# Optimization experiments

Measured on AMD Instinct MI355X. Metric: run time of the kernel, lower is better.

Reference implementation:

```python
import jax, jax.numpy as jnp
from jax import lax
import numpy as np

DN = ('NCHW', 'OIHW', 'NCHW')

def conv(x, w, b, stride=1, groups=1):
    y = lax.conv_general_dilated(x, w, (stride, stride), 'SAME',
                                 feature_group_count=groups, dimension_numbers=DN)
    return y + b[None, :, None, None]

def sep_conv(x, dw, pw, pb):
    # depthwise 3x3 -> pointwise 1x1 -> ReLU (BN is frozen at identity)
    y = lax.conv_general_dilated(x, dw, (1, 1), 'SAME',
                                 feature_group_count=x.shape[1], dimension_numbers=DN)
    return jax.nn.relu(conv(y, pw, pb))

def up2(x):
    return jnp.repeat(jnp.repeat(x, 2, axis=2), 2, axis=3)

def down2(x):
    return lax.reduce_window(x, -jnp.inf, lax.max, (1, 1, 2, 2), (1, 1, 2, 2), 'VALID')

def fuse(w, *xs):
    # fast normalized fusion
    w = jax.nn.relu(w)
    w = w / (jnp.sum(w) + 1e-4)
    out = w[0] * xs[0]
    for i in range(1, len(xs)):
        out = out + w[i] * xs[i]
    return out

def bifpn_layer(ps, dw, pw, pb, fw2, fw3):
    p3, p4, p5, p6, p7 = ps
    p6t = sep_conv(fuse(fw2[0], p6, up2(p7)),  dw[0], pw[0], pb[0])
    p5t = sep_conv(fuse(fw2[1], p5, up2(p6t)), dw[1], pw[1], pb[1])
    p4t = sep_conv(fuse(fw2[2], p4, up2(p5t)), dw[2], pw[2], pb[2])
    p3o = sep_conv(fuse(fw2[3], p3, up2(p4t)), dw[3], pw[3], pb[3])
    p4o = sep_conv(fuse(fw3[0], p4, p4t, down2(p3o)), dw[4], pw[4], pb[4])
    p5o = sep_conv(fuse(fw3[1], p5, p5t, down2(p4o)), dw[5], pw[5], pb[5])
    p6o = sep_conv(fuse(fw3[2], p6, p6t, down2(p5o)), dw[6], pw[6], pb[6])
    p7o = sep_conv(fuse(fw2[4], p7, down2(p6o)),      dw[7], pw[7], pb[7])
    return [p3o, p4o, p5o, p6o, p7o]

def make_anchors(img_size):
    # RetinaNet-style anchors: pyramid levels 3..7, 3 scales x 3 ratios
    ratios = np.array([0.5, 1.0, 2.0])
    scales = 2.0 ** (np.arange(3) / 3.0)
    boxes_all = []
    for lvl in range(3, 8):
        stride = 2 ** lvl
        size = 2 ** (lvl + 2)
        fs = img_size // stride
        ws = (size * scales[None, :] / np.sqrt(ratios)[:, None]).reshape(-1)  # [9]
        hs = (size * scales[None, :] * np.sqrt(ratios)[:, None]).reshape(-1)
        ctr = (np.arange(fs) + 0.5) * stride
        gy, gx = np.meshgrid(ctr, ctr, indexing='ij')
        centers = np.stack([gx, gy], -1).reshape(-1, 1, 2)      # [HW,1,2] (x,y)
        wh = np.stack([ws, hs], -1)[None]                       # [1,9,2]
        boxes = np.concatenate([centers - wh / 2, centers + wh / 2], -1).reshape(-1, 4)
        boxes_all.append(boxes)
    return jnp.asarray(np.concatenate(boxes_all, 0), jnp.float32)

def run_head(p, tw, tb, ow, ob, out_ch):
    x = p
    for i in range(tw.shape[0]):
        x = jax.nn.relu(conv(x, tw[i], tb[i]))
    y = conv(x, ow, ob)                                  # [B, 9*out_ch, H, W]
    B, _, H, W = y.shape
    return y.transpose(0, 2, 3, 1).reshape(B, H * W * 9, out_ch)

def setup_inputs() -> dict:
    key = jax.random.key(0)
    ks = iter(jax.random.split(key, 64))
    B, W, NC, ST, D = 4, 88, 90, 3, 4
    chans = [40, 80, 112, 192, 320]
    hw = [64, 32, 16, 8, 4]
    inp = {}
    for i, (c, h) in enumerate(zip(chans, hw)):
        inp[f'c{i+3}'] = jax.random.normal(next(ks), (B, c, h, h), jnp.float32)
        inp[f'lat_w{i+3}'] = jax.random.normal(next(ks), (W, c, 1, 1), jnp.float32) * 0.05
        inp[f'lat_b{i+3}'] = jnp.zeros((W,), jnp.float32)
    inp['bif_dw'] = jax.random.normal(next(ks), (ST, 8, W, 1, 3, 3), jnp.float32) * 0.1
    inp['bif_pw'] = jax.random.normal(next(ks), (ST, 8, W, W, 1, 1), jnp.float32) * 0.05
    inp['bif_pb'] = jnp.zeros((ST, 8, W), jnp.float32)
    inp['bif_fw2'] = jnp.ones((ST, 5, 2), jnp.float32)
    inp['bif_fw3'] = jnp.ones((ST, 3, 3), jnp.float32)
    inp['reg_tw'] = jax.random.normal(next(ks), (D, W, W, 3, 3), jnp.float32) * 0.03
    inp['reg_tb'] = jnp.zeros((D, W), jnp.float32)
    inp['reg_ow'] = jax.random.normal(next(ks), (36, W, 3, 3), jnp.float32) * 0.01
    inp['reg_ob'] = jnp.zeros((36,), jnp.float32)
    inp['cls_tw'] = jax.random.normal(next(ks), (D, W, W, 3, 3), jnp.float32) * 0.03
    inp['cls_tb'] = jnp.zeros((D, W), jnp.float32)
    inp['cls_ow'] = jax.random.normal(next(ks), (9 * NC, W, 3, 3), jnp.float32) * 0.01
    inp['cls_ob'] = jnp.full((9 * NC,), -np.log((1.0 - 0.01) / 0.01), jnp.float32)
    inp['img_size'] = 512
    return inp

def reference(c3, c4, c5, c6, c7,
              lat_w3, lat_b3, lat_w4, lat_b4, lat_w5, lat_b5,
              lat_w6, lat_b6, lat_w7, lat_b7,
              bif_dw, bif_pw, bif_pb, bif_fw2, bif_fw3,
              reg_tw, reg_tb, reg_ow, reg_ob,
              cls_tw, cls_tb, cls_ow, cls_ob,
              img_size):
    num_classes = cls_ow.shape[0] // 9
    ps = [conv(c3, lat_w3, lat_b3), conv(c4, lat_w4, lat_b4), conv(c5, lat_w5, lat_b5),
          conv(c6, lat_w6, lat_b6), conv(c7, lat_w7, lat_b7)]
    for s in range(bif_dw.shape[0]):
        ps = bifpn_layer(ps, bif_dw[s], bif_pw[s], bif_pb[s], bif_fw2[s], bif_fw3[s])
    regression = jnp.concatenate([run_head(p, reg_tw, reg_tb, reg_ow, reg_ob, 4) for p in ps], axis=1)
    classification = jnp.concatenate(
        [jax.nn.sigmoid(run_head(p, cls_tw, cls_tb, cls_ow, cls_ob, num_classes)) for p in ps], axis=1)
    anchors = make_anchors(int(img_size))
    return classification, regression, anchors
```

## Files before the change

### kernel.cpp

```cpp
#include <hip/hip_runtime.h>
#include <math.h>

#define TPB 256
static inline int cdiv(int a, int b) { return (a + b - 1) / b; }

typedef __attribute__((ext_vector_type(8))) short short8;
typedef __attribute__((ext_vector_type(4))) float floatx4;

__device__ __forceinline__ float bf2f(ushort u) {
    union { unsigned int u; float f; } v; v.u = ((unsigned int)u) << 16; return v.f;
}
__device__ __forceinline__ ushort f2bf(float f) {
    union { float f; unsigned int u; } v; v.f = f;
    unsigned int r = (v.u + 0x7FFFu + ((v.u >> 16) & 1u)) >> 16;
    return (ushort)r;
}

#define CONC_ROWS 21824
__device__ __forceinline__ void lvl_of(int row, int& lvl, int& base) {
    lvl = 0; base = 0;
    if (row >= 16384) { lvl = 1; base = 16384; }
    if (row >= 20480) { lvl = 2; base = 20480; }
    if (row >= 21504) { lvl = 3; base = 21504; }
    if (row >= 21760) { lvl = 4; base = 21760; }
}
__constant__ int LOFFc[5] = {0, 36864, 46080, 48384, 48960};

__global__ void pack3_k(const float* __restrict__ w, ushort* __restrict__ Bp,
                        int Ntot, int CO, int total) {
    int idx = blockIdx.x * blockDim.x + threadIdx.x;
    if (idx >= total) return;
    int j = idx & 7; int t = idx >> 3;
    int n = t % Ntot; t /= Ntot;
    int g = t & 3; t >>= 2;
    int ks = t % 3; int tap = t / 3;
    int ci = ks * 32 + g * 8 + j;
    float v = (ci < 88 && n < CO) ? w[((size_t)n * 88 + ci) * 9 + tap] : 0.f;
    Bp[idx] = f2bf(v);
}

__global__ void pack_tw8_k(const float* __restrict__ rw, const float* __restrict__ cw,
                           ushort* __restrict__ Bp) {
    int idx = blockIdx.x * blockDim.x + threadIdx.x;
    if (idx >= 8 * 82944) return;
    int i = idx / 82944; int r = idx - i * 82944;
    const float* w = (i < 4) ? rw + (size_t)i * 69696 : cw + (size_t)(i - 4) * 69696;
    int j = r & 7; int t = r >> 3;
    int n = t % 96; t /= 96;
    int g = t & 3; t >>= 2;
    int ks = t % 3; int tap = t / 3;
    int ci = ks * 32 + g * 8 + j;
    float v = (ci < 88 && n < 88) ? w[((size_t)n * 88 + ci) * 9 + tap] : 0.f;
    Bp[idx] = f2bf(v);
}

__global__ void pack_pw_all_k(const float* __restrict__ pw, ushort* __restrict__ Bp,
                              int total) {
    int idx = blockIdx.x * blockDim.x + threadIdx.x;
    if (idx >= total) return;
    int cid = idx / 9216; int r = idx - cid * 9216;
    int j = r & 7; int t = r >> 3;
    int n = t % 96; t /= 96;
    int g = t & 3; int ks = t >> 2;
    int ci = ks * 32 + g * 8 + j;
    float v = (ci < 88 && n < 88) ? pw[(size_t)cid * 7744 + n * 88 + ci] : 0.f;
    Bp[idx] = f2bf(v);
}

__global__ void pack_lat_k(const float* __restrict__ w3, const float* __restrict__ w4,
                           const float* __restrict__ w5, const float* __restrict__ w6,
                           const float* __restrict__ w7, ushort* __restrict__ Bp) {
    int idx = blockIdx.x * blockDim.x + threadIdx.x;
    if (idx >= 76800) return;
    int l, off;
    if (idx < 6144)       { l = 0; off = 0; }
    else if (idx < 15360) { l = 1; off = 6144; }
    else if (idx < 27648) { l = 2; off = 15360; }
    else if (idx < 46080) { l = 3; off = 27648; }
    else                  { l = 4; off = 46080; }
    const float* w = l == 0 ? w3 : l == 1 ? w4 : l == 2 ? w5 : l == 3 ? w6 : w7;
    const int cins[5] = {40, 80, 112, 192, 320};
    int Cin = cins[l];
    int r = idx - off;
    int j = r & 7; int t = r >> 3;
    int n = t % 96; t /= 96;
    int g = t & 3; int ks = t >> 2;
    int ci = ks * 32 + g * 8 + j;
    float v = (ci < Cin && n < 88) ? w[(size_t)n * Cin + ci] : 0.f;
    Bp[idx] = f2bf(v);
}

__global__ __launch_bounds__(256)
void lateral_mfma_k(const float* __restrict__ x, const ushort* __restrict__ Bp,
                    const float* __restrict__ bias, ushort* __restrict__ out,
                    int Cin, int KS, int logHH) {
    __shared__ ushort As[64 * 40];
    int tid = threadIdx.x;
    int m0 = blockIdx.x * 64;
    int lane = tid & 63, l15 = lane & 15, g = (lane >> 4) & 3;
    int wave = tid >> 6, wm = wave & 1, wn = wave >> 1;
    floatx4 acc[2][3];
#pragma unroll
    for (int a = 0; a < 2; ++a)
#pragma unroll
        for (int b = 0; b < 3; ++b) acc[a][b] = (floatx4){0.f, 0.f, 0.f, 0.f};
    const short8* Bq = (const short8*)Bp;

    int p = m0 + lane;
    int n = p >> logHH, pp = p & ((1 << logHH) - 1);
    const float* xp = x + (((size_t)n * Cin) << logHH) + pp;

    for (int ks = 0; ks < KS; ++ks) {
        __syncthreads();
#pragma unroll
        for (int it = 0; it < 8; ++it) {
            int ciL = (tid >> 6) + it * 4;
            int ci = ks * 32 + ciL;
            float v = (ci < Cin) ? xp[(size_t)ci << logHH] : 0.f;
            As[lane * 40 + ciL] = f2bf(v);
        }
        __syncthreads();
        short8 a0 = *(const short8*)(&As[(wm * 32 + l15) * 40 + g * 8]);
        short8 a1 = *(const short8*)(&As[(wm * 32 + 16 + l15) * 40 + g * 8]);
        int bbase = (ks * 4 + g) * 96 + wn * 48 + l15;
#pragma unroll
        for (int nf = 0; nf < 3; ++nf) {
            short8 b = Bq[bbase + nf * 16];
            acc[0][nf] = __builtin_amdgcn_mfma_f32_16x16x32_bf16(a0, b, acc[0][nf], 0, 0, 0);
            acc[1][nf] = __builtin_amdgcn_mfma_f32_16x16x32_bf16(a1, b, acc[1][nf], 0, 0, 0);
        }
    }
    float bc[3];
#pragma unroll
    for (int nf = 0; nf < 3; ++nf) {
        int c = wn * 48 + nf * 16 + l15;
        bc[nf] = (c < 88) ? bias[c] : 0.f;
    }
#pragma unroll
    for (int mf = 0; mf < 2; ++mf)
#pragma unroll
        for (int r = 0; r < 4; ++r) {
            int pl = m0 + wm * 32 + mf * 16 + g * 4 + r;
#pragma unroll
            for (int nf = 0; nf < 3; ++nf) {
                int c = wn * 48 + nf * 16 + l15;
                out[(size_t)pl * 96 + c] = f2bf(acc[mf][nf][r] + bc[nf]);
            }
        }
}

template <int MODE>
__global__ __launch_bounds__(256, 2)
void sepconv_k(const ushort* __restrict__ a, const ushort* __restrict__ bsrc,
               const ushort* __restrict__ csrc, const float* __restrict__ fw,
               const float* __restrict__ dww, const ushort* __restrict__ Bp,
               const float* __restrict__ pbias, ushort* __restrict__ out,
               int logW) {
    __shared__ ushort Fs[195 * 104];
    __shared__ ushort Ds[64 * 104];
    __shared__ ushort Dwb[108 * 8];
    int tid = threadIdx.x;
    int W = 1 << logW, HH = W * W, log2HH = 2 * logW;
    int Mlv = 4 * HH;
    int HB = W + 1;
    int RS = 64 + 2 * HB;
    int pl0 = blockIdx.x * 64;
    float w0 = fmaxf(fw[0], 0.f), w1 = fmaxf(fw[1], 0.f);
    float w2 = (MODE == 2) ? fmaxf(fw[2], 0.f) : 0.f;
    float inv = 1.f / (w0 + w1 + w2 + 1e-4f);
    float w0i = w0 * inv, w1i = w1 * inv, w2i = w2 * inv;

    if (tid < 13) *(uint4*)(&Fs[194 * 104 + tid * 8]) = (uint4){0u, 0u, 0u, 0u};
    for (int i = tid; i < 108; i += 256) {
        int cg = i / 9, tap = i - cg * 9;
        ushort tmp[8];
#pragma unroll
        for (int j = 0; j < 8; ++j) {
            int c = cg * 8 + j;
            tmp[j] = (c < 88) ? f2bf(dww[c * 9 + tap]) : (ushort)0;
        }
        *(uint4*)(&Dwb[i * 8]) = *(uint4*)tmp;
    }
    for (int i = tid; i < RS * 12; i += 256) {
        int row = i / 12, cg = i - row * 12;
        int pl = pl0 - HB + row;
        uint4 res = {0u, 0u, 0u, 0u};
        if (pl >= 0 && pl < Mlv) {
            int n = pl >> log2HH, pp = pl & (HH - 1);
            int y = pp >> logW, x = pp & (W - 1);
            uint4 av = *(const uint4*)(a + (size_t)pl * 96 + cg * 8);
            const ushort* au = (const ushort*)&av;
            float f[8];
            if (MODE == 0) {
                int Wh = W >> 1;
                int bp = (n << (log2HH - 2)) + (y >> 1) * Wh + (x >> 1);
                uint4 bv = *(const uint4*)(bsrc + (size_t)bp * 96 + cg * 8);
                const ushort* bu = (const ushort*)&bv;
#pragma unroll
                for (int j = 0; j < 8; ++j)
                    f[j] = w0i * bf2f(au[j]) + w1i * bf2f(bu[j]);
            } else {
                int W2 = W << 1;
                const ushort* q = (MODE == 1 ? bsrc : csrc) +
                    ((size_t)((n << (log2HH + 2)) + (2 * y) * W2 + 2 * x)) * 96 + cg * 8;
                uint4 q0 = *(const uint4*)(q);
                uint4 q1 = *(const uint4*)(q + 96);
                uint4 q2 = *(const uint4*)(q + (size_t)W2 * 96);
                uint4 q3 = *(const uint4*)(q + (size_t)W2 * 96 + 96);
                const ushort* u0 = (const ushort*)&q0; const ushort* u1 = (const ushort*)&q1;
                const ushort* u2 = (const ushort*)&q2; const ushort* u3 = (const ushort*)&q3;
                if (MODE == 1) {
#pragma unroll
                    for (int j = 0; j < 8; ++j) {
                        float m = fmaxf(fmaxf(bf2f(u0[j]), bf2f(u1[j])),
                                        fmaxf(bf2f(u2[j]), bf2f(u3[j])));
                        f[j] = w0i * bf2f(au[j]) + w1i * m;
                    }
                } else {
                    uint4 b2v = *(const uint4*)(bsrc + (size_t)pl * 96 + cg * 8);
                    const ushort* b2u = (const ushort*)&b2v;
#pragma unroll
                    for (int j = 0; j < 8; ++j) {
                        float m = fmaxf(fmaxf(bf2f(u0[j]), bf2f(u1[j])),
                                        fmaxf(bf2f(u2[j]), bf2f(u3[j])));
                        f[j] = w0i * bf2f(au[j]) + w1i * bf2f(b2u[j]) + w2i * m;
                    }
                }
            }
            ushort tmp[8];
#pragma unroll
            for (int j = 0; j < 8; ++j) tmp[j] = f2bf(f[j]);
            res = *(uint4*)tmp;
        }
        *(uint4*)(&Fs[row * 104 + cg * 8]) = res;
    }
    __syncthreads();
    for (int i = tid; i < 768; i += 256) {
        int row = i / 12, cg = i - row * 12;
        int pl = pl0 + row;
        int pp = pl & (HH - 1);
        int y = pp >> logW, x = pp & (W - 1);
        float acc8[8] = {0.f, 0.f, 0.f, 0.f, 0.f, 0.f, 0.f, 0.f};
        if (cg < 11) {
#pragma unroll
            for (int tap = 0; tap < 9; ++tap) {
                int dy = tap / 3 - 1, dx = tap % 3 - 1;
                int sy = y + dy, sx = x + dx;
                bool pred = ((unsigned)sy < (unsigned)W) && ((unsigned)sx < (unsigned)W);
                int rsel = pred ? (row + HB + dy * W + dx) : 194;
                short8 fv = *(const short8*)(&Fs[rsel * 104 + cg * 8]);
                short8 wv = *(const short8*)(&Dwb[(cg * 9 + tap) * 8]);
#pragma unroll
                for (int j = 0; j < 8; ++j)
                    acc8[j] = fmaf(bf2f((ushort)fv[j]), bf2f((ushort)wv[j]), acc8[j]);
            }
        }
        ushort tmp[8];
#pragma unroll
        for (int j = 0; j < 8; ++j) tmp[j] = f2bf(acc8[j]);
        *(uint4*)(&Ds[row * 104 + cg * 8]) = *(uint4*)tmp;
    }
    __syncthreads();
    int lane = tid & 63, l15 = lane & 15, g = (lane >> 4) & 3;
    int wave = tid >> 6, wm = wave & 1, wn = wave >> 1;
    floatx4 acc[2][3];
#pragma unroll
    for (int aa = 0; aa < 2; ++aa)
#pragma unroll
        for (int bb = 0; bb < 3; ++bb) acc[aa][bb] = (floatx4){0.f, 0.f, 0.f, 0.f};
    const short8* Bq = (const short8*)Bp;
#pragma unroll
    for (int ks = 0; ks < 3; ++ks) {
        int k = ks * 32 + g * 8;
        short8 a0 = *(const short8*)(&Ds[(wm * 32 + l15) * 104 + k]);
        short8 a1 = *(const short8*)(&Ds[(wm * 32 + 16 + l15) * 104 + k]);
        int bbase = (ks * 4 + g) * 96 + wn * 48 + l15;
#pragma unroll
        for (int nf = 0; nf < 3; ++nf) {
            short8 b = Bq[bbase + nf * 16];
            acc[0][nf] = __builtin_amdgcn_mfma_f32_16x16x32_bf16(a0, b, acc[0][nf], 0, 0, 0);
            acc[1][nf] = __builtin_amdgcn_mfma_f32_16x16x32_bf16(a1, b, acc[1][nf], 0, 0, 0);
        }
    }
    float bc[3];
#pragma unroll
    for (int nf = 0; nf < 3; ++nf) {
        int c = wn * 48 + nf * 16 + l15;
        bc[nf] = (c < 88) ? pbias[c] : 0.f;
    }
#pragma unroll
    for (int mf = 0; mf < 2; ++mf)
#pragma unroll
        for (int r = 0; r < 4; ++r) {
            int pl = pl0 + wm * 32 + mf * 16 + g * 4 + r;
#pragma unroll
            for (int nf = 0; nf < 3; ++nf) {
                int c = wn * 48 + nf * 16 + l15;
                out[(size_t)pl * 96 + c] = f2bf(fmaxf(acc[mf][nf][r] + bc[nf], 0.f));
            }
        }
}

__global__ __launch_bounds__(256)
void tower_direct_k(const ushort* __restrict__ inR, const ushort* __restrict__ inC,
                    const ushort* __restrict__ BpR, const ushort* __restrict__ BpC,
                    const float* __restrict__ bR, const float* __restrict__ bC,
                    ushort* __restrict__ outR, ushort* __restrict__ outC,
                    const ushort* __restrict__ zb) {
    int head = blockIdx.y;
    const ushort* in = head ? inC : inR;
    const short8* Bq = (const short8*)(head ? BpC : BpR);
    const float* bias = head ? bC : bR;
    ushort* out = head ? outC : outR;
    int tid = threadIdx.x;
    int m0 = blockIdx.x * 64;
    int lvl, base; lvl_of(m0, lvl, base);
    int logW = 6 - lvl, W = 1 << logW, HH = W * W;
    int pl0 = m0 - base;
    int lane = tid & 63, l15 = lane & 15, g = (lane >> 4) & 3;
    int wave = tid >> 6, wm = wave & 1, wn = wave >> 1;
    int ym[2], xm[2];
    const ushort* pbase[2];
#pragma unroll
    for (int mf = 0; mf < 2; ++mf) {
        int pl = pl0 + wm * 32 + mf * 16 + l15;
        int pp = pl & (HH - 1);
        ym[mf] = pp >> logW; xm[mf] = pp & (W - 1);
        pbase[mf] = in + (size_t)(base + pl) * 96 + g * 8;
    }
    const ushort* zbg = zb + g * 8;
    floatx4 acc[2][3];
#pragma unroll
    for (int aa = 0; aa < 2; ++aa)
#pragma unroll
        for (int bb = 0; bb < 3; ++bb) acc[aa][bb] = (floatx4){0.f, 0.f, 0.f, 0.f};
#pragma unroll
    for (int tap = 0; tap < 9; ++tap) {
        const int dy = tap / 3 - 1, dx = tap % 3 - 1;
        int off96 = (dy * W + dx) * 96;
        const ushort* ap[2];
#pragma unroll
        for (int mf = 0; mf < 2; ++mf) {
            bool pred = ((unsigned)(ym[mf] + dy) < (unsigned)W) &&
                        ((unsigned)(xm[mf] + dx) < (unsigned)W);
            ap[mf] = pred ? (pbase[mf] + off96) : zbg;
        }
#pragma unroll
        for (int ks = 0; ks < 3; ++ks) {
            short8 a0 = *(const short8*)(ap[0] + ks * 32);
            short8 a1 = *(const short8*)(ap[1] + ks * 32);
            int bbase = ((tap * 3 + ks) * 4 + g) * 96 + wn * 48 + l15;
#pragma unroll
            for (int nf = 0; nf < 3; ++nf) {
                short8 b = Bq[bbase + nf * 16];
                acc[0][nf] = __builtin_amdgcn_mfma_f32_16x16x32_bf16(a0, b, acc[0][nf], 0, 0, 0);
                acc[1][nf] = __builtin_amdgcn_mfma_f32_16x16x32_bf16(a1, b, acc[1][nf], 0, 0, 0);
            }
        }
    }
    float bc[3];
#pragma unroll
    for (int nf = 0; nf < 3; ++nf) {
        int c = wn * 48 + nf * 16 + l15;
        bc[nf] = (c < 88) ? bias[c] : 0.f;
    }
#pragma unroll
    for (int mf = 0; mf < 2; ++mf)
#pragma unroll
        for (int r = 0; r < 4; ++r) {
            int pl = pl0 + wm * 32 + mf * 16 + g * 4 + r;
#pragma unroll
            for (int nf = 0; nf < 3; ++nf) {
                int c = wn * 48 + nf * 16 + l15;
                out[(size_t)(base + pl) * 96 + c] = f2bf(fmaxf(acc[mf][nf][r] + bc[nf], 0.f));
            }
        }
}

template <int OC, bool SIG>
__global__ __launch_bounds__(256)
void head_direct_k(const ushort* __restrict__ in, const ushort* __restrict__ Bp,
                   const float* __restrict__ bias, float* __restrict__ outb,
                   int Ntot, int C9, const ushort* __restrict__ zb) {
    int tid = threadIdx.x;
    int m0 = blockIdx.x * 64;
    int n0b = blockIdx.y * 96;
    int lvl, base; lvl_of(m0, lvl, base);
    int logW = 6 - lvl, W = 1 << logW, HH = W * W, log2HH = 2 * logW;
    int pl0 = m0 - base;
    int lane = tid & 63, l15 = lane & 15, g = (lane >> 4) & 3;
    int wave = tid >> 6, wm = wave & 1, wn = wave >> 1;
    int ym[2], xm[2];
    const ushort* pbase[2];
#pragma unroll
    for (int mf = 0; mf < 2; ++mf) {
        int pl = pl0 + wm * 32 + mf * 16 + l15;
        int pp = pl & (HH - 1);
        ym[mf] = pp >> logW; xm[mf] = pp & (W - 1);
        pbase[mf] = in + (size_t)(base + pl) * 96 + g * 8;
    }
    const ushort* zbg = zb + g * 8;
    floatx4 acc[2][3];
#pragma unroll
    for (int aa = 0; aa < 2; ++aa)
#pragma unroll
        for (int bb = 0; bb < 3; ++bb) acc[aa][bb] = (floatx4){0.f, 0.f, 0.f, 0.f};
    const short8* Bq = (const short8*)Bp;
#pragma unroll
    for (int tap = 0; tap < 9; ++tap) {
        const int dy = tap / 3 - 1, dx = tap % 3 - 1;
        int off96 = (dy * W + dx) * 96;
        const ushort* ap[2];
#pragma unroll
        for (int mf = 0; mf < 2; ++mf) {
            bool pred = ((unsigned)(ym[mf] + dy) < (unsigned)W) &&
                        ((unsigned)(xm[mf] + dx) < (unsigned)W);
            ap[mf] = pred ? (pbase[mf] + off96) : zbg;
        }
#pragma unroll
        for (int ks = 0; ks < 3; ++ks) {
            short8 a0 = *(const short8*)(ap[0] + ks * 32);
            short8 a1 = *(const short8*)(ap[1] + ks * 32);
            int bbase = ((tap * 3 + ks) * 4 + g) * Ntot + n0b + wn * 48 + l15;
#pragma unroll
            for (int nf = 0; nf < 3; ++nf) {
                short8 b = Bq[bbase + nf * 16];
                acc[0][nf] = __builtin_amdgcn_mfma_f32_16x16x32_bf16(a0, b, acc[0][nf], 0, 0, 0);
                acc[1][nf] = __builtin_amdgcn_mfma_f32_16x16x32_bf16(a1, b, acc[1][nf], 0, 0, 0);
            }
        }
    }
#pragma unroll
    for (int nf = 0; nf < 3; ++nf) {
        int c = n0b + wn * 48 + nf * 16 + l15;
        if (c >= C9) continue;
        float bcv = bias[c];
        int a = c / OC, kk = c - a * OC;
#pragma unroll
        for (int mf = 0; mf < 2; ++mf)
#pragma unroll
            for (int r = 0; r < 4; ++r) {
                int pl = pl0 + wm * 32 + mf * 16 + g * 4 + r;
                int n = pl >> log2HH, pp = pl & (HH - 1);
                float v = acc[mf][nf][r] + bcv;
                if (SIG) v = 1.f / (1.f + expf(-v));
                outb[((size_t)n * 49104 + LOFFc[lvl] + (size_t)pp * 9 + a) * OC + kk] = v;
            }
    }
}

__global__ void anchors_k(float* __restrict__ out, ushort* __restrict__ zb) {
    int idx = blockIdx.x * blockDim.x + threadIdx.x;
    if (idx < 48) ((unsigned int*)zb)[idx] = 0u;
    if (idx >= 49104) return;
    const int offs[6] = {0, 36864, 46080, 48384, 48960, 49104};
    int l = 0;
    while (idx >= offs[l + 1]) ++l;
    int j = idx - offs[l];
    int a = j % 9;
    int p = j / 9;
    int fs = 64 >> l;
    int stride = 8 << l;
    float size = (float)(32 << l);
    int ix = p % fs, iy = p / fs;
    float cx = (ix + 0.5f) * (float)stride;
    float cy = (iy + 0.5f) * (float)stride;
    const float scl[3] = {1.0f, 1.2599210498948732f, 1.5874010519681994f};
    const float sqr[3] = {0.7071067811865476f, 1.0f, 1.4142135623730951f};
    int r = a / 3, s = a % 3;
    float w = size * scl[s] / sqr[r];
    float h = size * scl[s] * sqr[r];
    float* o = out + (size_t)idx * 4;
    o[0] = cx - 0.5f * w;
    o[1] = cy - 0.5f * h;
    o[2] = cx + 0.5f * w;
    o[3] = cy + 0.5f * h;
}


extern "C" void kernel_launch(void* const* d_in, const int* in_sizes, int n_in,
                              void* d_out, int out_size, void* d_ws, size_t ws_size,
                              hipStream_t stream) {
    const float* c_in[5]  = {(const float*)d_in[0],  (const float*)d_in[3],
                             (const float*)d_in[6],  (const float*)d_in[9],
                             (const float*)d_in[12]};
    const float* lat_w[5] = {(const float*)d_in[1],  (const float*)d_in[4],
                             (const float*)d_in[7],  (const float*)d_in[10],
                             (const float*)d_in[13]};
    const float* lat_b[5] = {(const float*)d_in[2],  (const float*)d_in[5],
                             (const float*)d_in[8],  (const float*)d_in[11],
                             (const float*)d_in[14]};
    const float* bif_dw  = (const float*)d_in[15];
    const float* bif_pw  = (const float*)d_in[16];
    const float* bif_pb  = (const float*)d_in[17];
    const float* bif_fw2 = (const float*)d_in[18];
    const float* bif_fw3 = (const float*)d_in[19];
    const float* reg_tw  = (const float*)d_in[20];
    const float* reg_tb  = (const float*)d_in[21];
    const float* reg_ow  = (const float*)d_in[22];
    const float* reg_ob  = (const float*)d_in[23];
    const float* cls_tw  = (const float*)d_in[24];
    const float* cls_tb  = (const float*)d_in[25];
    const float* cls_ow  = (const float*)d_in[26];
    const float* cls_ob  = (const float*)d_in[27];

    const int CINL[5] = {40, 80, 112, 192, 320};
    const int KSL[5]  = {2, 3, 4, 6, 10};
    const int LATO[5] = {0, 6144, 15360, 27648, 46080};
    const int ROFF[5] = {0, 16384, 20480, 21504, 21760};
    const int ML[5]   = {16384, 4096, 1024, 256, 64};
    const size_t CONC = (size_t)CONC_ROWS * 96;

    ushort* ws = (ushort*)d_ws;
    size_t off = 0;
    ushort* CA = ws + off; off += CONC;
    ushort* CB = ws + off; off += CONC;
    ushort* T4 = ws + off; off += (size_t)4096 * 96;
    ushort* T5 = ws + off; off += (size_t)1024 * 96;
    ushort* T6 = ws + off; off += (size_t)256 * 96;
    ushort* HXR0 = ws + off; off += CONC;
    ushort* HXR1 = ws + off; off += CONC;
    ushort* HXC0 = ws + off; off += CONC;
    ushort* HXC1 = ws + off; off += CONC;
    ushort* BP_PW  = ws + off; off += (size_t)24 * 9216;
    ushort* BP_TW  = ws + off; off += (size_t)8 * 82944;
    ushort* BP_RO  = ws + off; off += (size_t)82944;
    ushort* BP_CO  = ws + off; off += (size_t)746496;
    ushort* BP_LAT = ws + off; off += (size_t)76800;
    ushort* ZB     = ws + off; off += 96;
    (void)ws_size; (void)n_in; (void)in_sizes; (void)out_size;

    pack_pw_all_k<<<cdiv(24 * 9216, TPB), TPB, 0, stream>>>(bif_pw, BP_PW, 24 * 9216);
    pack_tw8_k<<<cdiv(8 * 82944, TPB), TPB, 0, stream>>>(reg_tw, cls_tw, BP_TW);
    pack3_k<<<cdiv(82944, TPB), TPB, 0, stream>>>(reg_ow, BP_RO, 96, 36, 82944);
    pack3_k<<<cdiv(746496, TPB), TPB, 0, stream>>>(cls_ow, BP_CO, 864, 810, 746496);
    pack_lat_k<<<cdiv(76800, TPB), TPB, 0, stream>>>(
        lat_w[0], lat_w[1], lat_w[2], lat_w[3], lat_w[4], BP_LAT);

    float* cls_base = (float*)d_out;
    float* reg_base = cls_base + (size_t)4 * 49104 * 90;
    float* anc_base = reg_base + (size_t)4 * 49104 * 4;
    anchors_k<<<cdiv(49104, TPB), TPB, 0, stream>>>(anc_base, ZB);

    for (int l = 0; l < 5; ++l) {
        int logHH = 2 * (6 - l);
        lateral_mfma_k<<<ML[l] / 64, 256, 0, stream>>>(
            c_in[l], BP_LAT + LATO[l], lat_b[l], CA + (size_t)ROFF[l] * 96,
            CINL[l], KSL[l], logHH);
    }

    ushort* cur = CA; ushort* nxt = CB;
    for (int s = 0; s < 3; ++s) {
        const float* dws = bif_dw + (size_t)s * 8 * 792;
        const float* pbs = bif_pb + (size_t)s * 8 * 88;
        const float* f2  = bif_fw2 + (size_t)s * 10;
        const float* f3  = bif_fw3 + (size_t)s * 9;
        auto LP = [&](ushort* buf, int l) { return buf + (size_t)ROFF[l] * 96; };
        auto BPW = [&](int ci) { return BP_PW + (size_t)(s * 8 + ci) * 9216; };

        sepconv_k<0><<<ML[3] / 64, 256, 0, stream>>>(
            LP(cur, 3), LP(cur, 4), nullptr, f2 + 0, dws + 0 * 792, BPW(0), pbs + 0 * 88, T6, 3);
        sepconv_k<0><<<ML[2] / 64, 256, 0, stream>>>(
            LP(cur, 2), T6, nullptr, f2 + 2, dws + 1 * 792, BPW(1), pbs + 1 * 88, T5, 4);
        sepconv_k<0><<<ML[1] / 64, 256, 0, stream>>>(
            LP(cur, 1), T5, nullptr, f2 + 4, dws + 2 * 792, BPW(2), pbs + 2 * 88, T4, 5);
        sepconv_k<0><<<ML[0] / 64, 256, 0, stream>>>(
            LP(cur, 0), T4, nullptr, f2 + 6, dws + 3 * 792, BPW(3), pbs + 3 * 88, LP(nxt, 0), 6);
        sepconv_k<2><<<ML[1] / 64, 256, 0, stream>>>(
            LP(cur, 1), T4, LP(nxt, 0), f3 + 0, dws + 4 * 792, BPW(4), pbs + 4 * 88, LP(nxt, 1), 5);
        sepconv_k<2><<<ML[2] / 64, 256, 0, stream>>>(
            LP(cur, 2), T5, LP(nxt, 1), f3 + 3, dws + 5 * 792, BPW(5), pbs + 5 * 88, LP(nxt, 2), 4);
        sepconv_k<2><<<ML[3] / 64, 256, 0, stream>>>(
            LP(cur, 3), T6, LP(nxt, 2), f3 + 6, dws + 6 * 792, BPW(6), pbs + 6 * 88, LP(nxt, 3), 3);
        sepconv_k<1><<<ML[4] / 64, 256, 0, stream>>>(
            LP(cur, 4), LP(nxt, 3), nullptr, f2 + 8, dws + 7 * 792, BPW(7), pbs + 7 * 88, LP(nxt, 4), 2);

        ushort* tp = cur; cur = nxt; nxt = tp;
    }

    const int GB = CONC_ROWS / 64;
    ushort* hxr[2] = {HXR0, HXR1};
    ushort* hxc[2] = {HXC0, HXC1};
    const ushort* xr = cur;
    const ushort* xc = cur;
    for (int i = 0; i < 4; ++i) {
        tower_direct_k<<<dim3(GB, 2), 256, 0, stream>>>(
            xr, xc, BP_TW + (size_t)i * 82944, BP_TW + (size_t)(4 + i) * 82944,
            reg_tb + i * 88, cls_tb + i * 88, hxr[i & 1], hxc[i & 1], ZB);
        xr = hxr[i & 1]; xc = hxc[i & 1];
    }
    head_direct_k<4, false><<<dim3(GB, 1), 256, 0, stream>>>(
        xr, BP_RO, reg_ob, reg_base, 96, 36, ZB);
    head_direct_k<90, true><<<dim3(GB, 9), 256, 0, stream>>>(
        xc, BP_CO, cls_ob, cls_base, 864, 810, ZB);
}
```

Baseline: 688.2 us.

## Prefetch B fragments per tap, merge reg/cls output heads into one launch

The tower and output-head conv kernels now load the next tap's weight fragments into registers while the current tap's MFMAs run, and they issue all A loads for a tap before its MFMA chain. This is meant to hide global-load latency. The two output-head launches become a single kernel with a 10-wide grid.y, whose class path uses runtime OC and sigmoid instead of template parameters. Launch bounds now request 3 blocks per CU and the final outputs use nontemporal stores. The double-buffered B registers raise register pressure and may spill under the occupancy hint, and the runtime OC division makes index arithmetic more costly.

```diff
diff --git a/kernel.cpp b/kernel.cpp
--- a/kernel.cpp
+++ b/kernel.cpp
@@ -301,7 +301,7 @@
         }
 }
 
-__global__ __launch_bounds__(256)
+__global__ __launch_bounds__(256, 3)
 void tower_direct_k(const ushort* __restrict__ inR, const ushort* __restrict__ inC,
                     const ushort* __restrict__ BpR, const ushort* __restrict__ BpC,
                     const float* __restrict__ bR, const float* __restrict__ bC,
@@ -329,13 +329,31 @@
         pbase[mf] = in + (size_t)(base + pl) * 96 + g * 8;
     }
     const ushort* zbg = zb + g * 8;
+    int bcol = wn * 48 + l15;
+
     floatx4 acc[2][3];
 #pragma unroll
     for (int aa = 0; aa < 2; ++aa)
 #pragma unroll
         for (int bb = 0; bb < 3; ++bb) acc[aa][bb] = (floatx4){0.f, 0.f, 0.f, 0.f};
+
+    short8 Bc[3][3], Bn[3][3];
+#pragma unroll
+    for (int ks = 0; ks < 3; ++ks) {
+        int bb = (ks * 4 + g) * 96 + bcol;
+#pragma unroll
+        for (int nf = 0; nf < 3; ++nf) Bc[ks][nf] = Bq[bb + nf * 16];
+    }
 #pragma unroll
     for (int tap = 0; tap < 9; ++tap) {
+        if (tap < 8) {
+#pragma unroll
+            for (int ks = 0; ks < 3; ++ks) {
+                int bb = (((tap + 1) * 3 + ks) * 4 + g) * 96 + bcol;
+#pragma unroll
+                for (int nf = 0; nf < 3; ++nf) Bn[ks][nf] = Bq[bb + nf * 16];
+            }
+        }
         const int dy = tap / 3 - 1, dx = tap % 3 - 1;
         int off96 = (dy * W + dx) * 96;
         const ushort* ap[2];
@@ -345,17 +363,24 @@
                         ((unsigned)(xm[mf] + dx) < (unsigned)W);
             ap[mf] = pred ? (pbase[mf] + off96) : zbg;
         }
+        short8 A0[3], A1[3];
 #pragma unroll
         for (int ks = 0; ks < 3; ++ks) {
-            short8 a0 = *(const short8*)(ap[0] + ks * 32);
-            short8 a1 = *(const short8*)(ap[1] + ks * 32);
-            int bbase = ((tap * 3 + ks) * 4 + g) * 96 + wn * 48 + l15;
+            A0[ks] = *(const short8*)(ap[0] + ks * 32);
+            A1[ks] = *(const short8*)(ap[1] + ks * 32);
+        }
+#pragma unroll
+        for (int ks = 0; ks < 3; ++ks)
 #pragma unroll
             for (int nf = 0; nf < 3; ++nf) {
-                short8 b = Bq[bbase + nf * 16];
-                acc[0][nf] = __builtin_amdgcn_mfma_f32_16x16x32_bf16(a0, b, acc[0][nf], 0, 0, 0);
-                acc[1][nf] = __builtin_amdgcn_mfma_f32_16x16x32_bf16(a1, b, acc[1][nf], 0, 0, 0);
-            }
+                acc[0][nf] = __builtin_amdgcn_mfma_f32_16x16x32_bf16(A0[ks], Bc[ks][nf], acc[0][nf], 0, 0, 0);
+                acc[1][nf] = __builtin_amdgcn_mfma_f32_16x16x32_bf16(A1[ks], Bc[ks][nf], acc[1][nf], 0, 0, 0);
+            }
+        if (tap < 8) {
+#pragma unroll
+            for (int ks = 0; ks < 3; ++ks)
+#pragma unroll
+                for (int nf = 0; nf < 3; ++nf) Bc[ks][nf] = Bn[ks][nf];
         }
     }
     float bc[3];
@@ -377,14 +402,25 @@
         }
 }
 
-template <int OC, bool SIG>
-__global__ __launch_bounds__(256)
-void head_direct_k(const ushort* __restrict__ in, const ushort* __restrict__ Bp,
-                   const float* __restrict__ bias, float* __restrict__ outb,
-                   int Ntot, int C9, const ushort* __restrict__ zb) {
+__global__ __launch_bounds__(256, 3)
+void heads_out_k(const ushort* __restrict__ xr, const ushort* __restrict__ xc,
+                 const ushort* __restrict__ BpR, const ushort* __restrict__ BpC,
+                 const float* __restrict__ bR, const float* __restrict__ bC,
+                 float* __restrict__ outR, float* __restrict__ outC,
+                 const ushort* __restrict__ zb) {
+    int yb = blockIdx.y;
+    bool isReg = (yb == 0);
+    const ushort* in = isReg ? xr : xc;
+    const short8* Bq = (const short8*)(isReg ? BpR : BpC);
+    const float* bias = isReg ? bR : bC;
+    float* outb = isReg ? outR : outC;
+    const int Ntot = isReg ? 96 : 864;
+    const int C9 = isReg ? 36 : 810;
+    const int OC = isReg ? 4 : 90;
+    const int n0b = isReg ? 0 : (yb - 1) * 96;
+
     int tid = threadIdx.x;
     int m0 = blockIdx.x * 64;
-    int n0b = blockIdx.y * 96;
     int lvl, base; lvl_of(m0, lvl, base);
     int logW = 6 - lvl, W = 1 << logW, HH = W * W, log2HH = 2 * logW;
     int pl0 = m0 - base;
@@ -400,14 +436,31 @@
         pbase[mf] = in + (size_t)(base + pl) * 96 + g * 8;
     }
     const ushort* zbg = zb + g * 8;
+    int bcol = n0b + wn * 48 + l15;
+
     floatx4 acc[2][3];
 #pragma unroll
     for (int aa = 0; aa < 2; ++aa)
 #pragma unroll
         for (int bb = 0; bb < 3; ++bb) acc[aa][bb] = (floatx4){0.f, 0.f, 0.f, 0.f};
-    const short8* Bq = (const short8*)Bp;
+
+    short8 Bc[3][3], Bn[3][3];
+#pragma unroll
+    for (int ks = 0; ks < 3; ++ks) {
+        int bb = (ks * 4 + g) * Ntot + bcol;
+#pragma unroll
+        for (int nf = 0; nf < 3; ++nf) Bc[ks][nf] = Bq[bb + nf * 16];
+    }
 #pragma unroll
     for (int tap = 0; tap < 9; ++tap) {
+        if (tap < 8) {
+#pragma unroll
+            for (int ks = 0; ks < 3; ++ks) {
+                int bb = (((tap + 1) * 3 + ks) * 4 + g) * Ntot + bcol;
+#pragma unroll
+                for (int nf = 0; nf < 3; ++nf) Bn[ks][nf] = Bq[bb + nf * 16];
+            }
+        }
         const int dy = tap / 3 - 1, dx = tap % 3 - 1;
         int off96 = (dy * W + dx) * 96;
         const ushort* ap[2];
@@ -417,17 +470,24 @@
                         ((unsigned)(xm[mf] + dx) < (unsigned)W);
             ap[mf] = pred ? (pbase[mf] + off96) : zbg;
         }
+        short8 A0[3], A1[3];
 #pragma unroll
         for (int ks = 0; ks < 3; ++ks) {
-            short8 a0 = *(const short8*)(ap[0] + ks * 32);
-            short8 a1 = *(const short8*)(ap[1] + ks * 32);
-            int bbase = ((tap * 3 + ks) * 4 + g) * Ntot + n0b + wn * 48 + l15;
+            A0[ks] = *(const short8*)(ap[0] + ks * 32);
+            A1[ks] = *(const short8*)(ap[1] + ks * 32);
+        }
+#pragma unroll
+        for (int ks = 0; ks < 3; ++ks)
 #pragma unroll
             for (int nf = 0; nf < 3; ++nf) {
-                short8 b = Bq[bbase + nf * 16];
-                acc[0][nf] = __builtin_amdgcn_mfma_f32_16x16x32_bf16(a0, b, acc[0][nf], 0, 0, 0);
-                acc[1][nf] = __builtin_amdgcn_mfma_f32_16x16x32_bf16(a1, b, acc[1][nf], 0, 0, 0);
-            }
+                acc[0][nf] = __builtin_amdgcn_mfma_f32_16x16x32_bf16(A0[ks], Bc[ks][nf], acc[0][nf], 0, 0, 0);
+                acc[1][nf] = __builtin_amdgcn_mfma_f32_16x16x32_bf16(A1[ks], Bc[ks][nf], acc[1][nf], 0, 0, 0);
+            }
+        if (tap < 8) {
+#pragma unroll
+            for (int ks = 0; ks < 3; ++ks)
+#pragma unroll
+                for (int nf = 0; nf < 3; ++nf) Bc[ks][nf] = Bn[ks][nf];
         }
     }
 #pragma unroll
@@ -443,8 +503,9 @@
                 int pl = pl0 + wm * 32 + mf * 16 + g * 4 + r;
                 int n = pl >> log2HH, pp = pl & (HH - 1);
                 float v = acc[mf][nf][r] + bcv;
-                if (SIG) v = 1.f / (1.f + expf(-v));
-                outb[((size_t)n * 49104 + LOFFc[lvl] + (size_t)pp * 9 + a) * OC + kk] = v;
+                if (!isReg) v = 1.f / (1.f + expf(-v));
+                __builtin_nontemporal_store(
+                    v, &outb[((size_t)n * 49104 + LOFFc[lvl] + (size_t)pp * 9 + a) * OC + kk]);
             }
     }
 }
@@ -589,8 +650,6 @@
             reg_tb + i * 88, cls_tb + i * 88, hxr[i & 1], hxc[i & 1], ZB);
         xr = hxr[i & 1]; xc = hxc[i & 1];
     }
-    head_direct_k<4, false><<<dim3(GB, 1), 256, 0, stream>>>(
-        xr, BP_RO, reg_ob, reg_base, 96, 36, ZB);
-    head_direct_k<90, true><<<dim3(GB, 9), 256, 0, stream>>>(
-        xc, BP_CO, cls_ob, cls_base, 864, 810, ZB);
-}
+    heads_out_k<<<dim3(GB, 10), 256, 0, stream>>>(
+        xr, xc, BP_RO, BP_CO, reg_ob, cls_ob, reg_base, cls_base, ZB);
+}
```

New measurement: 724.8 us. +5.3%, slower.

## Stage conv weights through double-buffered LDS via async global-to-LDS loads

Applied to the files above, without the earlier changes.

The tower and head 3x3 conv kernels now copy each tap's packed weight slab into shared memory with global_load_lds, double-buffered so the next tap loads while the current tap's MFMAs run. The class-head weights are repacked into contiguous per-96-channel blocks so each block stages one slab per tap, and the regression and classification heads are merged into a single launch. The aim is to cut repeated global/L2 weight traffic and exposed load latency. In exchange it adds a block barrier per tap and 36 KB of LDS per block, which may reduce occupancy.

```diff
diff --git a/kernel.cpp b/kernel.cpp
--- a/kernel.cpp
+++ b/kernel.cpp
@@ -25,6 +25,14 @@
     if (row >= 21760) { lvl = 4; base = 21760; }
 }
 __constant__ int LOFFc[5] = {0, 36864, 46080, 48384, 48960};
+
+#define BSLAB 9216
+
+__device__ __forceinline__ void gld_lds16(const ushort* g, ushort* l) {
+    __builtin_amdgcn_global_load_lds(
+        (const __attribute__((address_space(1))) unsigned int*)g,
+        (__attribute__((address_space(3))) unsigned int*)l, 16, 0, 0);
+}
 
 __global__ void pack3_k(const float* __restrict__ w, ushort* __restrict__ Bp,
                         int Ntot, int CO, int total) {
@@ -36,6 +44,20 @@
     int ks = t % 3; int tap = t / 3;
     int ci = ks * 32 + g * 8 + j;
     float v = (ci < 88 && n < CO) ? w[((size_t)n * 88 + ci) * 9 + tap] : 0.f;
+    Bp[idx] = f2bf(v);
+}
+
+__global__ void pack_cls_k(const float* __restrict__ w, ushort* __restrict__ Bp) {
+    int idx = blockIdx.x * blockDim.x + threadIdx.x;
+    if (idx >= 746496) return;
+    int j = idx & 7; int t = idx >> 3;
+    int n = t % 96; t /= 96;
+    int g = t & 3; t >>= 2;
+    int ks = t % 3; t /= 3;
+    int tap = t % 9; int nb = t / 9;
+    int ci = ks * 32 + g * 8 + j;
+    int co = nb * 96 + n;
+    float v = (ci < 88 && co < 810) ? w[((size_t)co * 88 + ci) * 9 + tap] : 0.f;
     Bp[idx] = f2bf(v);
 }
 
@@ -58,7 +80,7 @@
                               int total) {
     int idx = blockIdx.x * blockDim.x + threadIdx.x;
     if (idx >= total) return;
-    int cid = idx / 9216; int r = idx - cid * 9216;
+    int cid = idx / BSLAB; int r = idx - cid * BSLAB;
     int j = r & 7; int t = r >> 3;
     int n = t % 96; t /= 96;
     int g = t & 3; int ks = t >> 2;
@@ -302,14 +324,15 @@
 }
 
 __global__ __launch_bounds__(256)
-void tower_direct_k(const ushort* __restrict__ inR, const ushort* __restrict__ inC,
-                    const ushort* __restrict__ BpR, const ushort* __restrict__ BpC,
-                    const float* __restrict__ bR, const float* __restrict__ bC,
-                    ushort* __restrict__ outR, ushort* __restrict__ outC,
-                    const ushort* __restrict__ zb) {
+void tower_pipe_k(const ushort* __restrict__ inR, const ushort* __restrict__ inC,
+                  const ushort* __restrict__ BpR, const ushort* __restrict__ BpC,
+                  const float* __restrict__ bR, const float* __restrict__ bC,
+                  ushort* __restrict__ outR, ushort* __restrict__ outC,
+                  const ushort* __restrict__ zb) {
+    __shared__ __align__(16) ushort Bs[2][BSLAB];
     int head = blockIdx.y;
     const ushort* in = head ? inC : inR;
-    const short8* Bq = (const short8*)(head ? BpC : BpR);
+    const ushort* Bg = head ? BpC : BpR;
     const float* bias = head ? bC : bR;
     ushort* out = head ? outC : outR;
     int tid = threadIdx.x;
@@ -329,13 +352,30 @@
         pbase[mf] = in + (size_t)(base + pl) * 96 + g * 8;
     }
     const ushort* zbg = zb + g * 8;
+    int fragoff = (g * 96 + wn * 48 + l15) * 8;
+
+    auto stage = [&](int tap) {
+        const ushort* src = Bg + tap * BSLAB;
+        ushort* dst = (ushort*)Bs[tap & 1];
+#pragma unroll
+        for (int it = 0; it < 5; ++it) {
+            int c = tid + it * 256;
+            if (c < 1152) gld_lds16(src + (size_t)c * 8, dst + (size_t)c * 8);
+        }
+    };
+
     floatx4 acc[2][3];
 #pragma unroll
     for (int aa = 0; aa < 2; ++aa)
 #pragma unroll
         for (int bb = 0; bb < 3; ++bb) acc[aa][bb] = (floatx4){0.f, 0.f, 0.f, 0.f};
+
+    stage(0);
+    __syncthreads();
 #pragma unroll
     for (int tap = 0; tap < 9; ++tap) {
+        if (tap < 8) stage(tap + 1);
+        const ushort* Bb = (const ushort*)Bs[tap & 1];
         const int dy = tap / 3 - 1, dx = tap % 3 - 1;
         int off96 = (dy * W + dx) * 96;
         const ushort* ap[2];
@@ -349,14 +389,15 @@
         for (int ks = 0; ks < 3; ++ks) {
             short8 a0 = *(const short8*)(ap[0] + ks * 32);
             short8 a1 = *(const short8*)(ap[1] + ks * 32);
-            int bbase = ((tap * 3 + ks) * 4 + g) * 96 + wn * 48 + l15;
+            const ushort* bb = Bb + ks * 3072 + fragoff;
 #pragma unroll
             for (int nf = 0; nf < 3; ++nf) {
-                short8 b = Bq[bbase + nf * 16];
+                short8 b = *(const short8*)(bb + nf * 128);
                 acc[0][nf] = __builtin_amdgcn_mfma_f32_16x16x32_bf16(a0, b, acc[0][nf], 0, 0, 0);
                 acc[1][nf] = __builtin_amdgcn_mfma_f32_16x16x32_bf16(a1, b, acc[1][nf], 0, 0, 0);
             }
         }
+        __syncthreads();
     }
     float bc[3];
 #pragma unroll
@@ -377,14 +418,25 @@
         }
 }
 
-template <int OC, bool SIG>
 __global__ __launch_bounds__(256)
-void head_direct_k(const ushort* __restrict__ in, const ushort* __restrict__ Bp,
-                   const float* __restrict__ bias, float* __restrict__ outb,
-                   int Ntot, int C9, const ushort* __restrict__ zb) {
+void heads_pipe_k(const ushort* __restrict__ xr, const ushort* __restrict__ xc,
+                  const ushort* __restrict__ BpR, const ushort* __restrict__ BpC,
+                  const float* __restrict__ bR, const float* __restrict__ bC,
+                  float* __restrict__ outR, float* __restrict__ outC,
+                  const ushort* __restrict__ zb) {
+    __shared__ __align__(16) ushort Bs[2][BSLAB];
+    int yb = blockIdx.y;
+    bool isReg = (yb == 0);
+    const ushort* in = isReg ? xr : xc;
+    const ushort* Bg = isReg ? BpR : (BpC + (size_t)(yb - 1) * 9 * BSLAB);
+    const float* bias = isReg ? bR : bC;
+    float* outb = isReg ? outR : outC;
+    const int C9 = isReg ? 36 : 810;
+    const int OC = isReg ? 4 : 90;
+    const int n0b = isReg ? 0 : (yb - 1) * 96;
+
     int tid = threadIdx.x;
     int m0 = blockIdx.x * 64;
-    int n0b = blockIdx.y * 96;
     int lvl, base; lvl_of(m0, lvl, base);
     int logW = 6 - lvl, W = 1 << logW, HH = W * W, log2HH = 2 * logW;
     int pl0 = m0 - base;
@@ -400,14 +452,30 @@
         pbase[mf] = in + (size_t)(base + pl) * 96 + g * 8;
     }
     const ushort* zbg = zb + g * 8;
+    int fragoff = (g * 96 + wn * 48 + l15) * 8;
+
+    auto stage = [&](int tap) {
+        const ushort* src = Bg + tap * BSLAB;
+        ushort* dst = (ushort*)Bs[tap & 1];
+#pragma unroll
+        for (int it = 0; it < 5; ++it) {
+            int c = tid + it * 256;
+            if (c < 1152) gld_lds16(src + (size_t)c * 8, dst + (size_t)c * 8);
+        }
+    };
+
     floatx4 acc[2][3];
 #pragma unroll
     for (int aa = 0; aa < 2; ++aa)
 #pragma unroll
         for (int bb = 0; bb < 3; ++bb) acc[aa][bb] = (floatx4){0.f, 0.f, 0.f, 0.f};
-    const short8* Bq = (const short8*)Bp;
+
+    stage(0);
+    __syncthreads();
 #pragma unroll
     for (int tap = 0; tap < 9; ++tap) {
+        if (tap < 8) stage(tap + 1);
+        const ushort* Bb = (const ushort*)Bs[tap & 1];
         const int dy = tap / 3 - 1, dx = tap % 3 - 1;
         int off96 = (dy * W + dx) * 96;
         const ushort* ap[2];
@@ -421,14 +489,15 @@
         for (int ks = 0; ks < 3; ++ks) {
             short8 a0 = *(const short8*)(ap[0] + ks * 32);
             short8 a1 = *(const short8*)(ap[1] + ks * 32);
-            int bbase = ((tap * 3 + ks) * 4 + g) * Ntot + n0b + wn * 48 + l15;
+            const ushort* bb = Bb + ks * 3072 + fragoff;
 #pragma unroll
             for (int nf = 0; nf < 3; ++nf) {
-                short8 b = Bq[bbase + nf * 16];
+                short8 b = *(const short8*)(bb + nf * 128);
                 acc[0][nf] = __builtin_amdgcn_mfma_f32_16x16x32_bf16(a0, b, acc[0][nf], 0, 0, 0);
                 acc[1][nf] = __builtin_amdgcn_mfma_f32_16x16x32_bf16(a1, b, acc[1][nf], 0, 0, 0);
             }
         }
+        __syncthreads();
     }
 #pragma unroll
     for (int nf = 0; nf < 3; ++nf) {
@@ -443,7 +512,7 @@
                 int pl = pl0 + wm * 32 + mf * 16 + g * 4 + r;
                 int n = pl >> log2HH, pp = pl & (HH - 1);
                 float v = acc[mf][nf][r] + bcv;
-                if (SIG) v = 1.f / (1.f + expf(-v));
+                if (!isReg) v = 1.f / (1.f + expf(-v));
                 outb[((size_t)n * 49104 + LOFFc[lvl] + (size_t)pp * 9 + a) * OC + kk] = v;
             }
     }
@@ -522,7 +591,7 @@
     ushort* HXR1 = ws + off; off += CONC;
     ushort* HXC0 = ws + off; off += CONC;
     ushort* HXC1 = ws + off; off += CONC;
-    ushort* BP_PW  = ws + off; off += (size_t)24 * 9216;
+    ushort* BP_PW  = ws + off; off += (size_t)24 * BSLAB;
     ushort* BP_TW  = ws + off; off += (size_t)8 * 82944;
     ushort* BP_RO  = ws + off; off += (size_t)82944;
     ushort* BP_CO  = ws + off; off += (size_t)746496;
@@ -530,10 +599,10 @@
     ushort* ZB     = ws + off; off += 96;
     (void)ws_size; (void)n_in; (void)in_sizes; (void)out_size;
 
-    pack_pw_all_k<<<cdiv(24 * 9216, TPB), TPB, 0, stream>>>(bif_pw, BP_PW, 24 * 9216);
+    pack_pw_all_k<<<cdiv(24 * BSLAB, TPB), TPB, 0, stream>>>(bif_pw, BP_PW, 24 * BSLAB);
     pack_tw8_k<<<cdiv(8 * 82944, TPB), TPB, 0, stream>>>(reg_tw, cls_tw, BP_TW);
     pack3_k<<<cdiv(82944, TPB), TPB, 0, stream>>>(reg_ow, BP_RO, 96, 36, 82944);
-    pack3_k<<<cdiv(746496, TPB), TPB, 0, stream>>>(cls_ow, BP_CO, 864, 810, 746496);
+    pack_cls_k<<<cdiv(746496, TPB), TPB, 0, stream>>>(cls_ow, BP_CO);
     pack_lat_k<<<cdiv(76800, TPB), TPB, 0, stream>>>(
         lat_w[0], lat_w[1], lat_w[2], lat_w[3], lat_w[4], BP_LAT);
 
@@ -556,7 +625,7 @@
         const float* f2  = bif_fw2 + (size_t)s * 10;
         const float* f3  = bif_fw3 + (size_t)s * 9;
         auto LP = [&](ushort* buf, int l) { return buf + (size_t)ROFF[l] * 96; };
-        auto BPW = [&](int ci) { return BP_PW + (size_t)(s * 8 + ci) * 9216; };
+        auto BPW = [&](int ci) { return BP_PW + (size_t)(s * 8 + ci) * BSLAB; };
 
         sepconv_k<0><<<ML[3] / 64, 256, 0, stream>>>(
             LP(cur, 3), LP(cur, 4), nullptr, f2 + 0, dws + 0 * 792, BPW(0), pbs + 0 * 88, T6, 3);
@@ -584,13 +653,11 @@
     const ushort* xr = cur;
     const ushort* xc = cur;
     for (int i = 0; i < 4; ++i) {
-        tower_direct_k<<<dim3(GB, 2), 256, 0, stream>>>(
+        tower_pipe_k<<<dim3(GB, 2), 256, 0, stream>>>(
             xr, xc, BP_TW + (size_t)i * 82944, BP_TW + (size_t)(4 + i) * 82944,
             reg_tb + i * 88, cls_tb + i * 88, hxr[i & 1], hxc[i & 1], ZB);
         xr = hxr[i & 1]; xc = hxc[i & 1];
     }
-    head_direct_k<4, false><<<dim3(GB, 1), 256, 0, stream>>>(
-        xr, BP_RO, reg_ob, reg_base, 96, 36, ZB);
-    head_direct_k<90, true><<<dim3(GB, 9), 256, 0, stream>>>(
-        xc, BP_CO, cls_ob, cls_base, 864, 810, ZB);
-}
+    heads_pipe_k<<<dim3(GB, 10), 256, 0, stream>>>(
+        xr, xc, BP_RO, BP_CO, reg_ob, cls_ob, reg_base, cls_base, ZB);
+}
```

Measured after the change: 647.9 us. -5.9%, faster.
